# Kernel tuning notes

Hardware: AMD Instinct MI355X
Metric: run time of the kernel (lower is better)

## Reference

```python
import jax, jax.numpy as jnp
import numpy as np

# quantization formats
E_Q, M_Q = 4, 3      # E4M3 fp8 for input/param quantizers
E_A, M_A = 5, 10     # fp16-like accumulate / output format


def quant(x, exp, man):
    """Round-to-nearest-even float quantization to (exp, man) bits,
    with subnormals and saturation (mptorch float_quantize semantics)."""
    ebias = 2 ** (exp - 1) - 1
    emin = 1 - ebias                      # min normal exponent
    maxv = (2.0 - 2.0 ** (-man)) * 2.0 ** ebias
    ax = jnp.abs(x)
    e = jnp.floor(jnp.log2(jnp.where(ax > 0, ax, 1.0)))
    e = jnp.maximum(e, emin)              # subnormal range shares emin scale
    scale = jnp.exp2(man - e)
    q = jnp.round(x * scale) / scale      # jnp.round is half-to-even
    return jnp.clip(q, -maxv, maxv)


def qgemm(x, wt, exp_add, man_add):
    """Custom-precision GEMM x[M,K] @ wt[K,N] with fma=True:
    the running accumulator is requantized to (exp_add, man_add)
    after every rank-1 (per-k) fused multiply-add."""
    M, K = x.shape
    N = wt.shape[1]

    def step(acc, xw):
        xk, wk = xw                       # [M], [N]
        acc = quant(acc + xk[:, None] * wk[None, :], exp_add, man_add)
        return acc, None

    acc0 = jnp.zeros((M, N), x.dtype)
    acc, _ = jax.lax.scan(step, acc0, (x.T, wt))
    return acc


def setup_inputs() -> dict:
    key = jax.random.key(0)
    k1, k2, k3 = jax.random.split(key, 3)
    in_f, out_f, m = 1024, 1024, 2048
    x = jax.random.normal(k1, (m, in_f), jnp.float32)
    weight = jax.random.normal(k2, (out_f, in_f), jnp.float32) / np.float32(np.sqrt(in_f))
    bound = 1.0 / np.float32(np.sqrt(in_f))
    bias = jax.random.uniform(k3, (out_f,), jnp.float32, -bound, bound)
    return {"x": x, "weight": weight, "bias": bias}


def reference(x, weight, bias):
    qx = quant(x, E_Q, M_Q)               # input_quant
    qw = quant(weight, E_Q, M_Q)          # param_quant
    qb = quant(bias, E_Q, M_Q)            # param_quant
    out = qgemm(qx, qw.T, E_A, M_A)       # float_gemm with fma accumulation
    out = out + qb[None, :]
    out = quant(out, E_A, M_A)            # output requantization
    return out
```

## Files before the change

### kernel.cpp

```cpp
#include <hip/hip_runtime.h>
#include <hip/hip_fp16.h>


#define M_DIM 2048
#define N_DIM 1024
#define K_DIM 1024

#define BM 64
#define BN 64
#define BK 64
#define NCHUNK (K_DIM / BK)

#define PKFMA_LO(acc, x, w) \
  asm("v_pk_fma_f16 %0, %1, %2, %0 op_sel:[0,0,0] op_sel_hi:[0,1,1]" \
      : "+v"(acc) : "v"(x), "v"(w))
#define PKFMA_HI(acc, x, w) \
  asm("v_pk_fma_f16 %0, %1, %2, %0 op_sel:[1,0,0] op_sel_hi:[1,1,1]" \
      : "+v"(acc) : "v"(x), "v"(w))

__device__ __forceinline__ float quant_e4m3(float v) {
  unsigned au = __float_as_uint(v) & 0x7fffffffu;
  if (au == 0u) return v;
  int e = (int)(au >> 23) - 127;
  if (e < -6) e = -6;
  float s  = __uint_as_float((unsigned)(130 - e) << 23);
  float is = __uint_as_float((unsigned)(124 + e) << 23);
  float r = rintf(v * s) * is;
  return fminf(240.f, fmaxf(-240.f, r));
}

__global__ __launch_bounds__(256) void prep_kernel(const float* __restrict__ x,
                                                   const float* __restrict__ w,
                                                   __half* __restrict__ xT,
                                                   __half* __restrict__ wT) {
  const int id = blockIdx.x;
  const float* in;
  __half* outp;
  int R, C, bx, by;
  if (id < 2048) { in = x; outp = xT; R = M_DIM; C = K_DIM; bx = id & 31; by = id >> 5; }
  else           { in = w; outp = wT; R = N_DIM; C = K_DIM; bx = (id - 2048) & 31; by = (id - 2048) >> 5; }

  __shared__ float tile[32][33];
  const int tx = threadIdx.x & 31;
  const int ty = threadIdx.x >> 5;
  const int c0 = bx * 32;
  const int r0 = by * 32;
#pragma unroll
  for (int i = 0; i < 4; i++) {
    int r = r0 + ty + i * 8;
    tile[ty + i * 8][tx] = quant_e4m3(in[(size_t)r * C + c0 + tx]);
  }
  __syncthreads();
#pragma unroll
  for (int i = 0; i < 4; i++) {
    int c = c0 + ty + i * 8;
    outp[(size_t)c * R + r0 + tx] = __float2half(tile[tx][ty + i * 8]);
  }
}

__global__ __launch_bounds__(256) void gemm_qfma(const __half* __restrict__ xT,
                                                 const __half* __restrict__ wT,
                                                 const float* __restrict__ b,
                                                 float* __restrict__ outp) {
  __shared__ __half xs[2][BK][BM];
  __shared__ __half wsh[2][BK][BN];

  const int tid = threadIdx.x;
  const int tn = tid & 15;
  const int tm = tid >> 4;
  const int tm4 = tm * 4, tn4 = tn * 4;
  const int bn0 = blockIdx.x * BN;
  const int bm0 = blockIdx.y * BM;

  unsigned acc[4][2];
#pragma unroll
  for (int i = 0; i < 4; i++)
#pragma unroll
    for (int j = 0; j < 2; j++) acc[i][j] = 0u;

  const int sr = tid >> 3, sc = (tid & 7) * 8;

  uint4 gx[2], gw[2];
#pragma unroll
  for (int p = 0; p < 2; p++) {
    gx[p] = *reinterpret_cast<const uint4*>(xT + (size_t)(sr + p * 32) * M_DIM + bm0 + sc);
    gw[p] = *reinterpret_cast<const uint4*>(wT + (size_t)(sr + p * 32) * N_DIM + bn0 + sc);
  }

  for (int c = 0; c < NCHUNK; c++) {
    const int buf = c & 1;
#pragma unroll
    for (int p = 0; p < 2; p++) {
      *reinterpret_cast<uint4*>(&xs[buf][sr + p * 32][sc]) = gx[p];
      *reinterpret_cast<uint4*>(&wsh[buf][sr + p * 32][sc]) = gw[p];
    }

    if (c + 1 < NCHUNK) {
      const int kn = (c + 1) * BK;
#pragma unroll
      for (int p = 0; p < 2; p++) {
        gx[p] = *reinterpret_cast<const uint4*>(xT + (size_t)(kn + sr + p * 32) * M_DIM + bm0 + sc);
        gw[p] = *reinterpret_cast<const uint4*>(wT + (size_t)(kn + sr + p * 32) * N_DIM + bn0 + sc);
      }
    }

    __syncthreads();

    const __half (*xsb)[BM] = xs[buf];
    const __half (*wsb)[BN] = wsh[buf];

    uint2 xv[4], wv[4];
#pragma unroll
    for (int s = 0; s < 3; s++) {
      xv[s] = *reinterpret_cast<const uint2*>(&xsb[s][tm4]);
      wv[s] = *reinterpret_cast<const uint2*>(&wsb[s][tn4]);
    }
#pragma unroll
    for (int kk = 0; kk < BK; kk++) {
      const int s = kk & 3;
      if (kk + 3 < BK) {
        const int sp = (kk + 3) & 3;
        xv[sp] = *reinterpret_cast<const uint2*>(&xsb[kk + 3][tm4]);
        wv[sp] = *reinterpret_cast<const uint2*>(&wsb[kk + 3][tn4]);
      }
      const unsigned x0 = xv[s].x, x1 = xv[s].y;
      const unsigned w0 = wv[s].x, w1 = wv[s].y;
      PKFMA_LO(acc[0][0], x0, w0); PKFMA_LO(acc[0][1], x0, w1);
      PKFMA_HI(acc[1][0], x0, w0); PKFMA_HI(acc[1][1], x0, w1);
      PKFMA_LO(acc[2][0], x1, w0); PKFMA_LO(acc[2][1], x1, w1);
      PKFMA_HI(acc[3][0], x1, w0); PKFMA_HI(acc[3][1], x1, w1);
    }
    __syncthreads();
  }

  float4 bq = *reinterpret_cast<const float4*>(b + bn0 + tn4);
  bq.x = quant_e4m3(bq.x); bq.y = quant_e4m3(bq.y);
  bq.z = quant_e4m3(bq.z); bq.w = quant_e4m3(bq.w);
#pragma unroll
  for (int i = 0; i < 4; i++) {
    float4 o;
    __half2 h0 = *reinterpret_cast<__half2*>(&acc[i][0]);
    __half2 h1 = *reinterpret_cast<__half2*>(&acc[i][1]);
    o.x = __half2float(__float2half(__low2float(h0)  + bq.x));
    o.y = __half2float(__float2half(__high2float(h0) + bq.y));
    o.z = __half2float(__float2half(__low2float(h1)  + bq.z));
    o.w = __half2float(__float2half(__high2float(h1) + bq.w));
    *reinterpret_cast<float4*>(outp + (size_t)(bm0 + tm4 + i) * N_DIM + bn0 + tn4) = o;
  }
}

extern "C" void kernel_launch(void* const* d_in, const int* in_sizes, int n_in,
                              void* d_out, int out_size, void* d_ws, size_t ws_size,
                              hipStream_t stream) {
  const float* x = (const float*)d_in[0];
  const float* w = (const float*)d_in[1];
  const float* b = (const float*)d_in[2];
  float* outp = (float*)d_out;

  char* ws = (char*)d_ws;
  __half* xT = (__half*)ws;
  __half* wT = (__half*)(ws + (size_t)(4 << 20));

  hipLaunchKernelGGL(prep_kernel, dim3(3072), dim3(256), 0, stream,
                     x, w, xT, wT);
  hipLaunchKernelGGL(gemm_qfma, dim3(N_DIM / BN, M_DIM / BM), dim3(256), 0, stream,
                     xT, wT, b, outp);
}
```

Before: 123.9 us.

## Drop transposes: row-major fp16 operands, x from global, padded W in LDS

```diff
diff --git a/kernel.cpp b/kernel.cpp
--- a/kernel.cpp
+++ b/kernel.cpp
@@ -9,6 +9,7 @@
 #define BM 64
 #define BN 64
 #define BK 64
+#define WPAD 72
 #define NCHUNK (K_DIM / BK)
 
 #define PKFMA_LO(acc, x, w) \
@@ -17,6 +18,13 @@
 #define PKFMA_HI(acc, x, w) \
   asm("v_pk_fma_f16 %0, %1, %2, %0 op_sel:[1,0,0] op_sel_hi:[1,1,1]" \
       : "+v"(acc) : "v"(x), "v"(w))
+
+__device__ __forceinline__ __half2 h2(unsigned u) {
+  __half2 r; *reinterpret_cast<unsigned*>(&r) = u; return r;
+}
+__device__ __forceinline__ unsigned u32(__half2 h) {
+  return *reinterpret_cast<unsigned*>(&h);
+}
 
 __device__ __forceinline__ float quant_e4m3(float v) {
   unsigned au = __float_as_uint(v) & 0x7fffffffu;
@@ -31,39 +39,27 @@
 
 __global__ __launch_bounds__(256) void prep_kernel(const float* __restrict__ x,
                                                    const float* __restrict__ w,
-                                                   __half* __restrict__ xT,
-                                                   __half* __restrict__ wT) {
-  const int id = blockIdx.x;
-  const float* in;
-  __half* outp;
-  int R, C, bx, by;
-  if (id < 2048) { in = x; outp = xT; R = M_DIM; C = K_DIM; bx = id & 31; by = id >> 5; }
-  else           { in = w; outp = wT; R = N_DIM; C = K_DIM; bx = (id - 2048) & 31; by = (id - 2048) >> 5; }
-
-  __shared__ float tile[32][33];
-  const int tx = threadIdx.x & 31;
-  const int ty = threadIdx.x >> 5;
-  const int c0 = bx * 32;
-  const int r0 = by * 32;
-#pragma unroll
-  for (int i = 0; i < 4; i++) {
-    int r = r0 + ty + i * 8;
-    tile[ty + i * 8][tx] = quant_e4m3(in[(size_t)r * C + c0 + tx]);
-  }
-  __syncthreads();
-#pragma unroll
-  for (int i = 0; i < 4; i++) {
-    int c = c0 + ty + i * 8;
-    outp[(size_t)c * R + r0 + tx] = __float2half(tile[tx][ty + i * 8]);
-  }
+                                                   __half* __restrict__ xq,
+                                                   __half* __restrict__ wq) {
+  const int bid = blockIdx.x;
+  const float* src;
+  __half* dst;
+  size_t base;
+  if (bid < 2048) { src = x; dst = xq; base = (size_t)bid * 1024; }
+  else            { src = w; dst = wq; base = (size_t)(bid - 2048) * 1024; }
+  const size_t idx = base + threadIdx.x * 4;
+  const float4 v = *reinterpret_cast<const float4*>(src + idx);
+  __half2 lo{__float2half(quant_e4m3(v.x)), __float2half(quant_e4m3(v.y))};
+  __half2 hi{__float2half(quant_e4m3(v.z)), __float2half(quant_e4m3(v.w))};
+  uint2 o{u32(lo), u32(hi)};
+  *reinterpret_cast<uint2*>(dst + idx) = o;
 }
 
-__global__ __launch_bounds__(256) void gemm_qfma(const __half* __restrict__ xT,
-                                                 const __half* __restrict__ wT,
+__global__ __launch_bounds__(256) void gemm_qfma(const __half* __restrict__ xq,
+                                                 const __half* __restrict__ wq,
                                                  const float* __restrict__ b,
                                                  float* __restrict__ outp) {
-  __shared__ __half xs[2][BK][BM];
-  __shared__ __half wsh[2][BK][BN];
+  __shared__ __half ws[2][BN][WPAD];
 
   const int tid = threadIdx.x;
   const int tn = tid & 15;
@@ -78,57 +74,74 @@
 #pragma unroll
     for (int j = 0; j < 2; j++) acc[i][j] = 0u;
 
-  const int sr = tid >> 3, sc = (tid & 7) * 8;
+  const __half* xb0 = xq + (size_t)(bm0 + tm4) * K_DIM;
+  const __half* xb1 = xq + (size_t)(bm0 + tm4 + 2) * K_DIM;
 
-  uint4 gx[2], gw[2];
+  const int srow = tid >> 3;
+  const int scol = (tid & 7) * 8;
+
+  uint4 gw[2];
 #pragma unroll
-  for (int p = 0; p < 2; p++) {
-    gx[p] = *reinterpret_cast<const uint4*>(xT + (size_t)(sr + p * 32) * M_DIM + bm0 + sc);
-    gw[p] = *reinterpret_cast<const uint4*>(wT + (size_t)(sr + p * 32) * N_DIM + bn0 + sc);
-  }
+  for (int p = 0; p < 2; p++)
+    gw[p] = *reinterpret_cast<const uint4*>(wq + (size_t)(bn0 + srow + p * 32) * K_DIM + scol);
+
+  uint4 xbuf[2][4], wbuf[2][4];
 
   for (int c = 0; c < NCHUNK; c++) {
     const int buf = c & 1;
+    const int k0 = c * BK;
 #pragma unroll
-    for (int p = 0; p < 2; p++) {
-      *reinterpret_cast<uint4*>(&xs[buf][sr + p * 32][sc]) = gx[p];
-      *reinterpret_cast<uint4*>(&wsh[buf][sr + p * 32][sc]) = gw[p];
+    for (int p = 0; p < 2; p++)
+      *reinterpret_cast<uint4*>(&ws[buf][srow + p * 32][scol]) = gw[p];
+    if (c + 1 < NCHUNK) {
+#pragma unroll
+      for (int p = 0; p < 2; p++)
+        gw[p] = *reinterpret_cast<const uint4*>(
+            wq + (size_t)(bn0 + srow + p * 32) * K_DIM + k0 + BK + scol);
     }
-
-    if (c + 1 < NCHUNK) {
-      const int kn = (c + 1) * BK;
-#pragma unroll
-      for (int p = 0; p < 2; p++) {
-        gx[p] = *reinterpret_cast<const uint4*>(xT + (size_t)(kn + sr + p * 32) * M_DIM + bm0 + sc);
-        gw[p] = *reinterpret_cast<const uint4*>(wT + (size_t)(kn + sr + p * 32) * N_DIM + bn0 + sc);
-      }
-    }
+    xbuf[0][0] = *reinterpret_cast<const uint4*>(xb0 + k0);
+    xbuf[0][1] = *reinterpret_cast<const uint4*>(xb0 + K_DIM + k0);
+    xbuf[0][2] = *reinterpret_cast<const uint4*>(xb1 + k0);
+    xbuf[0][3] = *reinterpret_cast<const uint4*>(xb1 + K_DIM + k0);
 
     __syncthreads();
 
-    const __half (*xsb)[BM] = xs[buf];
-    const __half (*wsb)[BN] = wsh[buf];
+#pragma unroll
+    for (int i = 0; i < 4; i++)
+      wbuf[0][i] = *reinterpret_cast<const uint4*>(&ws[buf][tn4 + i][0]);
 
-    uint2 xv[4], wv[4];
 #pragma unroll
-    for (int s = 0; s < 3; s++) {
-      xv[s] = *reinterpret_cast<const uint2*>(&xsb[s][tm4]);
-      wv[s] = *reinterpret_cast<const uint2*>(&wsb[s][tn4]);
-    }
+    for (int j = 0; j < 8; j++) {
+      const int cur = j & 1, nxt = cur ^ 1;
+      if (j < 7) {
+        const int kj = k0 + (j + 1) * 8;
+        xbuf[nxt][0] = *reinterpret_cast<const uint4*>(xb0 + kj);
+        xbuf[nxt][1] = *reinterpret_cast<const uint4*>(xb0 + K_DIM + kj);
+        xbuf[nxt][2] = *reinterpret_cast<const uint4*>(xb1 + kj);
+        xbuf[nxt][3] = *reinterpret_cast<const uint4*>(xb1 + K_DIM + kj);
 #pragma unroll
-    for (int kk = 0; kk < BK; kk++) {
-      const int s = kk & 3;
-      if (kk + 3 < BK) {
-        const int sp = (kk + 3) & 3;
-        xv[sp] = *reinterpret_cast<const uint2*>(&xsb[kk + 3][tm4]);
-        wv[sp] = *reinterpret_cast<const uint2*>(&wsb[kk + 3][tn4]);
+        for (int i = 0; i < 4; i++)
+          wbuf[nxt][i] = *reinterpret_cast<const uint4*>(&ws[buf][tn4 + i][(j + 1) * 8]);
       }
-      const unsigned x0 = xv[s].x, x1 = xv[s].y;
-      const unsigned w0 = wv[s].x, w1 = wv[s].y;
-      PKFMA_LO(acc[0][0], x0, w0); PKFMA_LO(acc[0][1], x0, w1);
-      PKFMA_HI(acc[1][0], x0, w0); PKFMA_HI(acc[1][1], x0, w1);
-      PKFMA_LO(acc[2][0], x1, w0); PKFMA_LO(acc[2][1], x1, w1);
-      PKFMA_HI(acc[3][0], x1, w0); PKFMA_HI(acc[3][1], x1, w1);
+#pragma unroll
+      for (int j2 = 0; j2 < 4; j2++) {
+        const unsigned A0 = (&wbuf[cur][0].x)[j2], B0 = (&wbuf[cur][1].x)[j2];
+        const unsigned A1 = (&wbuf[cur][2].x)[j2], B1 = (&wbuf[cur][3].x)[j2];
+        const unsigned we0 = u32(__lows2half2 (h2(A0), h2(B0)));
+        const unsigned we1 = u32(__lows2half2 (h2(A1), h2(B1)));
+        const unsigned wo0 = u32(__highs2half2(h2(A0), h2(B0)));
+        const unsigned wo1 = u32(__highs2half2(h2(A1), h2(B1)));
+        const unsigned x0 = (&xbuf[cur][0].x)[j2], x1 = (&xbuf[cur][1].x)[j2];
+        const unsigned x2 = (&xbuf[cur][2].x)[j2], x3 = (&xbuf[cur][3].x)[j2];
+        PKFMA_LO(acc[0][0], x0, we0); PKFMA_LO(acc[0][1], x0, we1);
+        PKFMA_LO(acc[1][0], x1, we0); PKFMA_LO(acc[1][1], x1, we1);
+        PKFMA_LO(acc[2][0], x2, we0); PKFMA_LO(acc[2][1], x2, we1);
+        PKFMA_LO(acc[3][0], x3, we0); PKFMA_LO(acc[3][1], x3, we1);
+        PKFMA_HI(acc[0][0], x0, wo0); PKFMA_HI(acc[0][1], x0, wo1);
+        PKFMA_HI(acc[1][0], x1, wo0); PKFMA_HI(acc[1][1], x1, wo1);
+        PKFMA_HI(acc[2][0], x2, wo0); PKFMA_HI(acc[2][1], x2, wo1);
+        PKFMA_HI(acc[3][0], x3, wo0); PKFMA_HI(acc[3][1], x3, wo1);
+      }
     }
     __syncthreads();
   }
@@ -138,9 +151,9 @@
   bq.z = quant_e4m3(bq.z); bq.w = quant_e4m3(bq.w);
 #pragma unroll
   for (int i = 0; i < 4; i++) {
+    const __half2 h0 = h2(acc[i][0]);
+    const __half2 h1 = h2(acc[i][1]);
     float4 o;
-    __half2 h0 = *reinterpret_cast<__half2*>(&acc[i][0]);
-    __half2 h1 = *reinterpret_cast<__half2*>(&acc[i][1]);
     o.x = __half2float(__float2half(__low2float(h0)  + bq.x));
     o.y = __half2float(__float2half(__high2float(h0) + bq.y));
     o.z = __half2float(__float2half(__low2float(h1)  + bq.z));
@@ -158,11 +171,11 @@
   float* outp = (float*)d_out;
 
   char* ws = (char*)d_ws;
-  __half* xT = (__half*)ws;
-  __half* wT = (__half*)(ws + (size_t)(4 << 20));
+  __half* xq = (__half*)ws;
+  __half* wq = (__half*)(ws + (size_t)(4 << 20));
 
   hipLaunchKernelGGL(prep_kernel, dim3(3072), dim3(256), 0, stream,
-                     x, w, xT, wT);
+                     x, w, xq, wq);
   hipLaunchKernelGGL(gemm_qfma, dim3(N_DIM / BN, M_DIM / BM), dim3(256), 0, stream,
-                     xT, wT, b, outp);
+                     xq, wq, b, outp);
 }
```

Result: slower. 130.6 us (+5.4%).
